# Optimization experiments

Measured on AMD Instinct MI355X. Metric: run time of the kernel, lower is better.

## Reference

```python
import jax, jax.numpy as jnp
import numpy as np

B = 32768
PASSES = 4

# mask layout: (batch, digit, row, col), values in {0,1}

def _to_lines(m, d):
    """Reorder so the last axis enumerates the 9 cells of a line and axis -2 the 9 lines."""
    if d == 'h':
        return m                      # lines = rows, cells = cols
    if d == 'v':
        return jnp.swapaxes(m, 2, 3)  # lines = cols, cells = rows
    b = m.shape[0]                    # lines = 3x3 boxes
    return m.reshape(b, 9, 3, 3, 3, 3).transpose(0, 1, 2, 4, 3, 5).reshape(b, 9, 9, 9)

_from_lines = _to_lines  # all three reorderings are self-inverse


def filter_line(m, d):
    """SudokuFilterHVBox: remove a solved cell's digit from all other cells in its line."""
    l = _to_lines(m, d)
    cnt = l.sum(axis=1, keepdims=True)                 # candidates per cell
    solved = l * (cnt == 1).astype(l.dtype)            # one-hot solved cells
    other = solved.sum(axis=-1, keepdims=True) - solved  # same digit solved elsewhere in line
    out = l * (other == 0).astype(l.dtype)
    return _from_lines(out, d)


def unique_line(m, d):
    """SudokuUniqueHVBox (hidden single): if a digit fits only one cell in a line, fix it."""
    l = _to_lines(m, d)
    cnt_line = l.sum(axis=-1, keepdims=True)           # per-digit count in the line
    hidden = l * (cnt_line == 1).astype(l.dtype)       # lone placements
    has = hidden.sum(axis=1, keepdims=True) > 0        # cell hosts a hidden single
    out = jnp.where(has, hidden, l)
    return _from_lines(out, d)


def doubles_line(m, d):
    """SudokuDigitsDoubles (naked pair): two identical 2-candidate cells in a line
    eliminate those digits from the rest of the line."""
    l = _to_lines(m, d)                                # (B, d, line, cell)
    cnt = l.sum(axis=1, keepdims=True)
    pm = l * (cnt == 2).astype(l.dtype)                # patterns of 2-candidate cells
    dot = jnp.einsum('bdlc,bdle->blce', pm, pm)        # pattern overlap between cells
    eye = jnp.eye(9, dtype=l.dtype)
    match = (dot == 2).astype(l.dtype) * (1.0 - eye)   # identical pair at another cell
    pairflag = match.sum(-1) > 0                       # (B, line, cell) part of a naked pair
    pair_digit = pm * pairflag[:, None, :, :].astype(l.dtype)
    total_pd = pair_digit.sum(-1, keepdims=True)       # digit belongs to some pair in line
    remove = (total_pd > 0) & (pair_digit == 0)
    out = l * (1.0 - remove.astype(l.dtype))
    return _from_lines(out, d)


def pointing(m, d):
    """SudokuDigitsInOneLineAtBox: if a digit's box candidates lie in one row/col,
    remove that digit from the rest of the row/col outside the box."""
    b = m.shape[0]
    v = m.reshape(b, 9, 3, 3, 3, 3)                    # (B, d, br, ri, bc, ci)
    if d == 'h':
        pres = v.sum(axis=5) > 0                       # (B,d,br,ri,bc) digit in row of box
        nrows = pres.sum(axis=3, keepdims=True)
        point = pres & (nrows == 1)                    # confined to single row within box
        tot = point.sum(axis=4, keepdims=True)         # over bc
        rem = (tot - point) > 0                        # pointing from another box hits us
        out = v * (1.0 - rem[..., None].astype(v.dtype))
    else:
        pres = v.sum(axis=3) > 0                       # (B,d,br,bc,ci) digit in col of box
        ncols = pres.sum(axis=4, keepdims=True)
        point = pres & (ncols == 1)
        tot = point.sum(axis=2, keepdims=True)         # over br
        rem = (tot - point) > 0
        out = v * (1.0 - rem[:, :, :, None, :, :].astype(v.dtype))
    return out.reshape(b, 9, 9, 9)


def _forward_mask(mask):
    for _ in range(PASSES):
        mask = filter_line(mask, 'box')
        mask = pointing(mask, 'h')
        mask = pointing(mask, 'v')
        mask = unique_line(mask, 'h')
        mask = unique_line(mask, 'v')
        mask = unique_line(mask, 'box')
        mask = doubles_line(mask, 'v')   # original code instantiates doubles_h with 'v'
        mask = doubles_line(mask, 'v')
        mask = doubles_line(mask, 'box')
    return mask


def setup_inputs() -> dict:
    key = jax.random.key(0)
    mask = jax.random.randint(key, (B, 9, 9, 9), 0, 2).astype(jnp.float32)
    return {"mask": mask}


def reference(mask):
    out = _forward_mask(mask)
    cnt = out.sum(axis=1)                              # candidates per cell
    solved = jnp.all(cnt == 1, axis=(1, 2))            # (B,) puzzle fully determined
    return (out, solved)
```

## Files before the change

kernel.cpp:

```cpp
#include <hip/hip_runtime.h>
#include <stdint.h>

#define NB 32768
#define NPASS 4
#define FULL27 0x07FFFFFFu
#define NBF (NB * 729)
#define PPW 16
#define NBLK (NB / PPW)
#define ROUNDS 183
#define POOLDW 368


__device__ __forceinline__ uint32_t colfold(uint32_t w) {
    return (w | (w >> 9) | (w >> 18)) & 0x1FFu;
}
__device__ __forceinline__ uint32_t colmaj2(uint32_t w) {
    return ((w & (w >> 9)) | ((w | (w >> 9)) & (w >> 18))) & 0x1FFu;
}
__device__ __forceinline__ uint32_t rotA(uint32_t v) {
    return (uint32_t)__builtin_amdgcn_update_dpp(0, (int)v, 0x09, 0xF, 0xF, true);
}
__device__ __forceinline__ uint32_t rotB(uint32_t v) {
    return (uint32_t)__builtin_amdgcn_update_dpp(0, (int)v, 0x12, 0xF, 0xF, true);
}

__global__ __launch_bounds__(64)
void sudoku_kernel(const uint32_t* __restrict__ in, float* __restrict__ out,
                   float* __restrict__ solved) {
    __shared__ uint32_t pool[POOLDW];
    const int lane = threadIdx.x;
    const int trip = lane >> 2;
    const int band = lane & 3;
    const int p0 = blockIdx.x * PPW;
    const int p = p0 + trip;

    {
        const int base = p0 * 729;
        #pragma unroll 1
        for (int c = 0; c < 11; ++c) {
            uint32_t v[16];
            #pragma unroll
            for (int j = 0; j < 16; ++j) {
                int gi = base + (c * 16 + j) * 64 + lane;
                if (gi >= NBF) gi = NBF - 1;
                v[j] = in[gi];
            }
            #pragma unroll
            for (int j = 0; j < 16; ++j) {
                unsigned long long m = __ballot(v[j] != 0u);
                if (lane == 0) {
                    int r = c * 16 + j;
                    pool[2 * r]     = (uint32_t)m;
                    pool[2 * r + 1] = (uint32_t)(m >> 32);
                }
            }
        }
        {
            uint32_t v[7];
            #pragma unroll
            for (int j = 0; j < 7; ++j) {
                int gi = base + (176 + j) * 64 + lane;
                if (gi >= NBF) gi = NBF - 1;
                v[j] = in[gi];
            }
            #pragma unroll
            for (int j = 0; j < 7; ++j) {
                unsigned long long m = __ballot(v[j] != 0u);
                if (lane == 0) {
                    int r = 176 + j;
                    pool[2 * r]     = (uint32_t)m;
                    pool[2 * r + 1] = (uint32_t)(m >> 32);
                }
            }
        }
    }
    __syncthreads();

    uint32_t bd[9];
    {
        const int bb0 = trip * 729 + band * 27;
        #pragma unroll
        for (int d = 0; d < 9; ++d) {
            int bb = bb0 + d * 81;
            int di = bb >> 5, sh = bb & 31;
            uint64_t both = (uint64_t)pool[di] | ((uint64_t)pool[di + 1] << 32);
            bd[d] = (uint32_t)(both >> sh) & FULL27;
        }
    }
    __syncthreads();

    #pragma unroll 1
    for (int pass = 0; pass < NPASS; ++pass) {
        {
            uint32_t on = 0, tw = 0, fo = 0;
            #pragma unroll
            for (int d = 0; d < 9; ++d) {
                uint32_t c = on & bd[d];
                on ^= bd[d]; fo |= tw & c; tw ^= c;
            }
            uint32_t ex1 = on & ~tw & ~fo;
            #pragma unroll
            for (int d = 0; d < 9; ++d) {
                uint32_t s = bd[d] & ex1;
                #pragma unroll
                for (int k = 0; k < 3; ++k) {
                    uint32_t bm = 0x1C0E07u << (3 * k);
                    uint32_t sm = s & bm;
                    uint32_t multi = sm & (sm - 1u);
                    uint32_t keep = (sm == 0u) ? 0xFFFFFFFFu : (~bm | (multi ? 0u : sm));
                    bd[d] &= keep;
                }
            }
        }

        #pragma unroll
        for (int d = 0; d < 9; ++d) {
            uint32_t w = bd[d];
            uint32_t t = (w | (w >> 1) | (w >> 2)) & 0x01249249u;
            uint32_t sum = (t & 0x1FFu) + ((t >> 9) & 0x1FFu) + ((t >> 18) & 0x1FFu);
            uint32_t single = sum & ~(sum >> 1) & 0x49u;
            uint32_t point = t & (single * 0x40201u);
            uint32_t clearm = 0;
            #pragma unroll
            for (int r = 0; r < 3; ++r) {
                uint32_t pr = (point >> (9 * r)) & 0x1FFu;
                uint32_t multi = pr & (pr - 1u);
                uint32_t segkeep = multi ? 0u : pr * 7u;
                uint32_t rc = pr ? ((0x1FFu & ~segkeep) << (9 * r)) : 0u;
                clearm |= rc;
            }
            bd[d] = w & ~clearm;
        }

        {
            uint32_t pnt[9];
            #pragma unroll
            for (int d = 0; d < 9; ++d) {
                uint32_t w = bd[d];
                uint32_t q = colfold(w);
                uint32_t u = (q & 0x49u) + ((q >> 1) & 0x49u) + ((q >> 2) & 0x49u);
                uint32_t single = u & ~(u >> 1) & 0x49u;
                pnt[d] = q & (single * 7u);
            }
            #pragma unroll
            for (int d = 0; d < 9; ++d) {
                uint32_t o = rotA(pnt[d]) | rotB(pnt[d]);
                bd[d] &= ~(o * 0x40201u);
            }
        }

        {
            uint32_t hid[9], has = 0;
            #pragma unroll
            for (int d = 0; d < 9; ++d) {
                uint32_t w = bd[d], h = 0;
                #pragma unroll
                for (int r = 0; r < 3; ++r) {
                    uint32_t x = w & (0x1FFu << (9 * r));
                    h |= (x & (x - 1u)) ? 0u : x;
                }
                hid[d] = h; has |= h;
            }
            #pragma unroll
            for (int d = 0; d < 9; ++d) bd[d] = (bd[d] & ~has) | hid[d];
        }

        {
            uint32_t hid[9], has = 0;
            #pragma unroll
            for (int d = 0; d < 9; ++d) {
                uint32_t w = bd[d];
                uint32_t q0 = colfold(w), m0 = colmaj2(w);
                uint32_t ex = q0 | (m0 << 9);
                uint32_t ea = rotA(ex);
                uint32_t eb = rotB(ex);
                uint32_t qa = ea & 0x1FFu, ma = ea >> 9;
                uint32_t qb = eb & 0x1FFu, mb = eb >> 9;
                uint32_t ge2 = m0 | ma | mb | (q0 & qa) | (q0 & qb) | (qa & qb);
                uint32_t ex1c = (q0 | qa | qb) & ~ge2;
                hid[d] = w & ((ex1c & q0) * 0x40201u);
                has |= hid[d];
            }
            #pragma unroll
            for (int d = 0; d < 9; ++d) bd[d] = (bd[d] & ~has) | hid[d];
        }

        {
            uint32_t hid[9], has = 0;
            #pragma unroll
            for (int d = 0; d < 9; ++d) {
                uint32_t w = bd[d], h = 0;
                #pragma unroll
                for (int k = 0; k < 3; ++k) {
                    uint32_t x = w & (0x1C0E07u << (3 * k));
                    h |= (x & (x - 1u)) ? 0u : x;
                }
                hid[d] = h; has |= h;
            }
            #pragma unroll
            for (int d = 0; d < 9; ++d) bd[d] = (bd[d] & ~has) | hid[d];
        }

        #pragma unroll 1
        for (int rep = 0; rep < 2; ++rep) {
            uint32_t on = 0, tw = 0, fo = 0;
            #pragma unroll
            for (int d = 0; d < 9; ++d) {
                uint32_t c = on & bd[d];
                on ^= bd[d]; fo |= tw & c; tw ^= c;
            }
            uint32_t ex2 = tw & ~on & ~fo;
            uint32_t Q[9], K[9];
            #pragma unroll
            for (int d = 0; d < 9; ++d) { Q[d] = bd[d] & ex2; K[d] = 0u; }
            #pragma unroll
            for (int d1 = 0; d1 < 9; ++d1)
                #pragma unroll
                for (int d2 = d1 + 1; d2 < 9; ++d2) {
                    uint32_t P = Q[d1] & Q[d2];
                    uint32_t f0 = colfold(P), g0 = colmaj2(P);
                    uint32_t ex = f0 | (g0 << 9);
                    uint32_t ea = rotA(ex);
                    uint32_t eb = rotB(ex);
                    uint32_t fa = ea & 0x1FFu, ga = ea >> 9;
                    uint32_t fb = eb & 0x1FFu, gb = eb >> 9;
                    uint32_t dup = g0 | ga | gb | (f0 & fa) | (f0 & fb) | (fa & fb);
                    uint32_t sK = P & (dup * 0x40201u);
                    K[d1] |= sK; K[d2] |= sK;
                }
            #pragma unroll
            for (int d = 0; d < 9; ++d) {
                uint32_t kc = colfold(K[d]);
                uint32_t cols = kc | rotA(kc) | rotB(kc);
                uint32_t em = cols * 0x40201u;
                bd[d] = (bd[d] & ~em) | K[d];
            }
        }

        {
            uint32_t on = 0, tw = 0, fo = 0;
            #pragma unroll
            for (int d = 0; d < 9; ++d) {
                uint32_t c = on & bd[d];
                on ^= bd[d]; fo |= tw & c; tw ^= c;
            }
            uint32_t ex2 = tw & ~on & ~fo;
            uint32_t Q[9], K[9];
            #pragma unroll
            for (int d = 0; d < 9; ++d) { Q[d] = bd[d] & ex2; K[d] = 0u; }
            #pragma unroll
            for (int d1 = 0; d1 < 9; ++d1)
                #pragma unroll
                for (int d2 = d1 + 1; d2 < 9; ++d2) {
                    uint32_t P = Q[d1] & Q[d2];
                    #pragma unroll
                    for (int k = 0; k < 3; ++k) {
                        uint32_t m = P & (0x1C0E07u << (3 * k));
                        uint32_t s = (m & (m - 1u)) ? m : 0u;
                        K[d1] |= s; K[d2] |= s;
                    }
                }
            #pragma unroll
            for (int d = 0; d < 9; ++d)
                #pragma unroll
                for (int k = 0; k < 3; ++k) {
                    uint32_t bm = 0x1C0E07u << (3 * k);
                    uint32_t t = K[d] & bm;
                    uint32_t mask = t ? (~bm | t) : 0xFFFFFFFFu;
                    bd[d] &= mask;
                }
        }
    }

    {
        uint32_t on = 0, tw = 0, fo = 0;
        #pragma unroll
        for (int d = 0; d < 9; ++d) {
            uint32_t c = on & bd[d];
            on ^= bd[d]; fo |= tw & c; tw ^= c;
        }
        uint32_t okb = ((on & ~tw & ~fo) == FULL27) ? 1u : 0u;
        uint32_t all = okb & rotA(okb) & rotB(okb);
        if (band == 0) solved[p] = all ? 1.0f : 0.0f;
    }

    for (int j = lane; j < POOLDW; j += 64) pool[j] = 0u;
    __syncthreads();
    if (band != 3) {
        const int pbit = trip * 729;
        #pragma unroll
        for (int d = 0; d < 9; ++d) {
            int bitbase = pbit + d * 81 + band * 27;
            int di = bitbase >> 5;
            int sh = bitbase & 31;
            uint64_t both = (uint64_t)bd[d] << sh;
            atomicOr(&pool[di], (uint32_t)both);
            atomicOr(&pool[di + 1], (uint32_t)(both >> 32));
        }
    }
    __syncthreads();
    {
        const int limit4 = PPW * 729 / 4;
        float4* dst4 = (float4*)(out + (size_t)p0 * 729);
        #pragma unroll 4
        for (int i = 0; i < 46; ++i) {
            int j = i * 64 + lane;
            if (j < limit4) {
                uint32_t nib = (pool[j >> 3] >> ((j & 7) * 4)) & 0xFu;
                dst4[j] = make_float4((float)(nib & 1u), (float)((nib >> 1) & 1u),
                                      (float)((nib >> 2) & 1u), (float)((nib >> 3) & 1u));
            }
        }
    }
}

extern "C" void kernel_launch(void* const* d_in, const int* in_sizes, int n_in,
                              void* d_out, int out_size, void* d_ws, size_t ws_size,
                              hipStream_t stream) {
    const uint32_t* in = (const uint32_t*)d_in[0];
    float* out = (float*)d_out;
    float* solved = out + (size_t)NB * 729;
    sudoku_kernel<<<NBLK, 64, 0, stream>>>(in, out, solved);
}
```

Before: 213.5 us.

## Split into bit-pack kernel and one-puzzle-per-lane solve kernel

Adds a separate pack kernel that reads the float mask with wide loads and packs it into a bitset workspace, so the input read is no longer done through per-block ballots. The solve kernel now gives each lane a whole puzzle, holding three bands in registers, which replaces the cross-lane DPP rotations with in-register indexing. Each lane now holds three times as much state, which raises register pressure and can limit occupancy. There are also only 512 blocks of 64 threads and a second kernel launch.

```diff
diff --git a/kernel.cpp b/kernel.cpp
--- a/kernel.cpp
+++ b/kernel.cpp
@@ -5,10 +5,11 @@
 #define NPASS 4
 #define FULL27 0x07FFFFFFu
 #define NBF (NB * 729)
-#define PPW 16
-#define NBLK (NB / PPW)
-#define ROUNDS 183
-#define POOLDW 368
+#define NWORDS (NBF / 32)
+#define PACK_BLKS (NWORDS / 256)
+#define SOLVE_PPB 64
+#define SOLVE_BLKS (NB / SOLVE_PPB)
+#define BLK_DW 1458
 
 
 __device__ __forceinline__ uint32_t colfold(uint32_t w) {
@@ -17,143 +18,124 @@
 __device__ __forceinline__ uint32_t colmaj2(uint32_t w) {
     return ((w & (w >> 9)) | ((w | (w >> 9)) & (w >> 18))) & 0x1FFu;
 }
-__device__ __forceinline__ uint32_t rotA(uint32_t v) {
-    return (uint32_t)__builtin_amdgcn_update_dpp(0, (int)v, 0x09, 0xF, 0xF, true);
-}
-__device__ __forceinline__ uint32_t rotB(uint32_t v) {
-    return (uint32_t)__builtin_amdgcn_update_dpp(0, (int)v, 0x12, 0xF, 0xF, true);
-}
-
-__global__ __launch_bounds__(64)
-void sudoku_kernel(const uint32_t* __restrict__ in, float* __restrict__ out,
-                   float* __restrict__ solved) {
-    __shared__ uint32_t pool[POOLDW];
+
+__global__ __launch_bounds__(256)
+void pack_kernel(const uint32_t* __restrict__ in, uint32_t* __restrict__ ws) {
+    const int g = blockIdx.x * 256 + threadIdx.x;
+    const uint4* src = (const uint4*)in + (size_t)g * 8;
+    uint32_t acc = 0u;
+    #pragma unroll
+    for (int j = 0; j < 8; ++j) {
+        uint4 v = src[j];
+        uint32_t n = ((v.x >> 23) & 1u) | (((v.y >> 23) & 1u) << 1)
+                   | (((v.z >> 23) & 1u) << 2) | (((v.w >> 23) & 1u) << 3);
+        acc |= n << (4 * j);
+    }
+    ws[g] = acc;
+}
+
+__global__ __launch_bounds__(64, 1)
+void solve_kernel(const uint32_t* __restrict__ ws, float* __restrict__ out,
+                  float* __restrict__ solved) {
+    __shared__ uint32_t lds[BLK_DW + 1];
     const int lane = threadIdx.x;
-    const int trip = lane >> 2;
-    const int band = lane & 3;
-    const int p0 = blockIdx.x * PPW;
-    const int p = p0 + trip;
-
-    {
-        const int base = p0 * 729;
-        #pragma unroll 1
-        for (int c = 0; c < 11; ++c) {
-            uint32_t v[16];
-            #pragma unroll
-            for (int j = 0; j < 16; ++j) {
-                int gi = base + (c * 16 + j) * 64 + lane;
-                if (gi >= NBF) gi = NBF - 1;
-                v[j] = in[gi];
-            }
-            #pragma unroll
-            for (int j = 0; j < 16; ++j) {
-                unsigned long long m = __ballot(v[j] != 0u);
-                if (lane == 0) {
-                    int r = c * 16 + j;
-                    pool[2 * r]     = (uint32_t)m;
-                    pool[2 * r + 1] = (uint32_t)(m >> 32);
-                }
-            }
-        }
-        {
-            uint32_t v[7];
-            #pragma unroll
-            for (int j = 0; j < 7; ++j) {
-                int gi = base + (176 + j) * 64 + lane;
-                if (gi >= NBF) gi = NBF - 1;
-                v[j] = in[gi];
-            }
-            #pragma unroll
-            for (int j = 0; j < 7; ++j) {
-                unsigned long long m = __ballot(v[j] != 0u);
-                if (lane == 0) {
-                    int r = 176 + j;
-                    pool[2 * r]     = (uint32_t)m;
-                    pool[2 * r + 1] = (uint32_t)(m >> 32);
-                }
-            }
+    const int P0 = blockIdx.x * SOLVE_PPB;
+
+    {
+        const uint2* wsrc = (const uint2*)(ws + (size_t)blockIdx.x * BLK_DW);
+        uint2* ldst = (uint2*)lds;
+        #pragma unroll
+        for (int i = 0; i < 12; ++i) {
+            int j = i * 64 + lane;
+            if (j < 729) ldst[j] = wsrc[j];
         }
     }
     __syncthreads();
 
-    uint32_t bd[9];
-    {
-        const int bb0 = trip * 729 + band * 27;
-        #pragma unroll
-        for (int d = 0; d < 9; ++d) {
-            int bb = bb0 + d * 81;
-            int di = bb >> 5, sh = bb & 31;
-            uint64_t both = (uint64_t)pool[di] | ((uint64_t)pool[di + 1] << 32);
-            bd[d] = (uint32_t)(both >> sh) & FULL27;
-        }
-    }
-    __syncthreads();
+    uint32_t bd[9][3];
+    {
+        const int qb = lane * 729;
+        #pragma unroll
+        for (int d = 0; d < 9; ++d)
+            #pragma unroll
+            for (int b = 0; b < 3; ++b) {
+                int bit = qb + d * 81 + b * 27;
+                int di = bit >> 5, sh = bit & 31;
+                uint64_t both = (uint64_t)lds[di] | ((uint64_t)lds[di + 1] << 32);
+                bd[d][b] = (uint32_t)(both >> sh) & FULL27;
+            }
+    }
 
     #pragma unroll 1
     for (int pass = 0; pass < NPASS; ++pass) {
-        {
+        #pragma unroll
+        for (int b = 0; b < 3; ++b) {
             uint32_t on = 0, tw = 0, fo = 0;
             #pragma unroll
             for (int d = 0; d < 9; ++d) {
-                uint32_t c = on & bd[d];
-                on ^= bd[d]; fo |= tw & c; tw ^= c;
+                uint32_t c = on & bd[d][b];
+                on ^= bd[d][b]; fo |= tw & c; tw ^= c;
             }
             uint32_t ex1 = on & ~tw & ~fo;
             #pragma unroll
             for (int d = 0; d < 9; ++d) {
-                uint32_t s = bd[d] & ex1;
+                uint32_t s = bd[d][b] & ex1;
                 #pragma unroll
                 for (int k = 0; k < 3; ++k) {
                     uint32_t bm = 0x1C0E07u << (3 * k);
                     uint32_t sm = s & bm;
                     uint32_t multi = sm & (sm - 1u);
                     uint32_t keep = (sm == 0u) ? 0xFFFFFFFFu : (~bm | (multi ? 0u : sm));
-                    bd[d] &= keep;
-                }
-            }
-        }
+                    bd[d][b] &= keep;
+                }
+            }
+        }
+
+        #pragma unroll
+        for (int b = 0; b < 3; ++b)
+            #pragma unroll
+            for (int d = 0; d < 9; ++d) {
+                uint32_t w = bd[d][b];
+                uint32_t t = (w | (w >> 1) | (w >> 2)) & 0x01249249u;
+                uint32_t sum = (t & 0x1FFu) + ((t >> 9) & 0x1FFu) + ((t >> 18) & 0x1FFu);
+                uint32_t single = sum & ~(sum >> 1) & 0x49u;
+                uint32_t point = t & (single * 0x40201u);
+                uint32_t clearm = 0;
+                #pragma unroll
+                for (int r = 0; r < 3; ++r) {
+                    uint32_t pr = (point >> (9 * r)) & 0x1FFu;
+                    uint32_t multi = pr & (pr - 1u);
+                    uint32_t segkeep = multi ? 0u : pr * 7u;
+                    uint32_t rc = pr ? ((0x1FFu & ~segkeep) << (9 * r)) : 0u;
+                    clearm |= rc;
+                }
+                bd[d][b] = w & ~clearm;
+            }
 
         #pragma unroll
         for (int d = 0; d < 9; ++d) {
-            uint32_t w = bd[d];
-            uint32_t t = (w | (w >> 1) | (w >> 2)) & 0x01249249u;
-            uint32_t sum = (t & 0x1FFu) + ((t >> 9) & 0x1FFu) + ((t >> 18) & 0x1FFu);
-            uint32_t single = sum & ~(sum >> 1) & 0x49u;
-            uint32_t point = t & (single * 0x40201u);
-            uint32_t clearm = 0;
-            #pragma unroll
-            for (int r = 0; r < 3; ++r) {
-                uint32_t pr = (point >> (9 * r)) & 0x1FFu;
-                uint32_t multi = pr & (pr - 1u);
-                uint32_t segkeep = multi ? 0u : pr * 7u;
-                uint32_t rc = pr ? ((0x1FFu & ~segkeep) << (9 * r)) : 0u;
-                clearm |= rc;
-            }
-            bd[d] = w & ~clearm;
-        }
-
-        {
-            uint32_t pnt[9];
-            #pragma unroll
-            for (int d = 0; d < 9; ++d) {
-                uint32_t w = bd[d];
+            uint32_t pn[3];
+            #pragma unroll
+            for (int b = 0; b < 3; ++b) {
+                uint32_t w = bd[d][b];
                 uint32_t q = colfold(w);
                 uint32_t u = (q & 0x49u) + ((q >> 1) & 0x49u) + ((q >> 2) & 0x49u);
                 uint32_t single = u & ~(u >> 1) & 0x49u;
-                pnt[d] = q & (single * 7u);
-            }
-            #pragma unroll
-            for (int d = 0; d < 9; ++d) {
-                uint32_t o = rotA(pnt[d]) | rotB(pnt[d]);
-                bd[d] &= ~(o * 0x40201u);
-            }
-        }
-
-        {
+                pn[b] = q & (single * 7u);
+            }
+            #pragma unroll
+            for (int b = 0; b < 3; ++b) {
+                uint32_t o = pn[(b + 1) % 3] | pn[(b + 2) % 3];
+                bd[d][b] &= ~(o * 0x40201u);
+            }
+        }
+
+        #pragma unroll
+        for (int b = 0; b < 3; ++b) {
             uint32_t hid[9], has = 0;
             #pragma unroll
             for (int d = 0; d < 9; ++d) {
-                uint32_t w = bd[d], h = 0;
+                uint32_t w = bd[d][b], h = 0;
                 #pragma unroll
                 for (int r = 0; r < 3; ++r) {
                     uint32_t x = w & (0x1FFu << (9 * r));
@@ -162,34 +144,41 @@
                 hid[d] = h; has |= h;
             }
             #pragma unroll
-            for (int d = 0; d < 9; ++d) bd[d] = (bd[d] & ~has) | hid[d];
+            for (int d = 0; d < 9; ++d) bd[d][b] = (bd[d][b] & ~has) | hid[d];
         }
 
         {
+            uint32_t hid[9][3], has[3] = {0u, 0u, 0u};
+            #pragma unroll
+            for (int d = 0; d < 9; ++d) {
+                uint32_t q[3], m[3];
+                #pragma unroll
+                for (int b = 0; b < 3; ++b) {
+                    q[b] = colfold(bd[d][b]);
+                    m[b] = colmaj2(bd[d][b]);
+                }
+                uint32_t ge2 = m[0] | m[1] | m[2]
+                             | (q[0] & q[1]) | (q[0] & q[2]) | (q[1] & q[2]);
+                uint32_t ex1c = (q[0] | q[1] | q[2]) & ~ge2;
+                #pragma unroll
+                for (int b = 0; b < 3; ++b) {
+                    hid[d][b] = bd[d][b] & ((ex1c & q[b]) * 0x40201u);
+                    has[b] |= hid[d][b];
+                }
+            }
+            #pragma unroll
+            for (int d = 0; d < 9; ++d)
+                #pragma unroll
+                for (int b = 0; b < 3; ++b)
+                    bd[d][b] = (bd[d][b] & ~has[b]) | hid[d][b];
+        }
+
+        #pragma unroll
+        for (int b = 0; b < 3; ++b) {
             uint32_t hid[9], has = 0;
             #pragma unroll
             for (int d = 0; d < 9; ++d) {
-                uint32_t w = bd[d];
-                uint32_t q0 = colfold(w), m0 = colmaj2(w);
-                uint32_t ex = q0 | (m0 << 9);
-                uint32_t ea = rotA(ex);
-                uint32_t eb = rotB(ex);
-                uint32_t qa = ea & 0x1FFu, ma = ea >> 9;
-                uint32_t qb = eb & 0x1FFu, mb = eb >> 9;
-                uint32_t ge2 = m0 | ma | mb | (q0 & qa) | (q0 & qb) | (qa & qb);
-                uint32_t ex1c = (q0 | qa | qb) & ~ge2;
-                hid[d] = w & ((ex1c & q0) * 0x40201u);
-                has |= hid[d];
-            }
-            #pragma unroll
-            for (int d = 0; d < 9; ++d) bd[d] = (bd[d] & ~has) | hid[d];
-        }
-
-        {
-            uint32_t hid[9], has = 0;
-            #pragma unroll
-            for (int d = 0; d < 9; ++d) {
-                uint32_t w = bd[d], h = 0;
+                uint32_t w = bd[d][b], h = 0;
                 #pragma unroll
                 for (int k = 0; k < 3; ++k) {
                     uint32_t x = w & (0x1C0E07u << (3 * k));
@@ -198,56 +187,69 @@
                 hid[d] = h; has |= h;
             }
             #pragma unroll
-            for (int d = 0; d < 9; ++d) bd[d] = (bd[d] & ~has) | hid[d];
+            for (int d = 0; d < 9; ++d) bd[d][b] = (bd[d][b] & ~has) | hid[d];
         }
 
         #pragma unroll 1
         for (int rep = 0; rep < 2; ++rep) {
+            uint32_t ex2[3];
+            #pragma unroll
+            for (int b = 0; b < 3; ++b) {
+                uint32_t on = 0, tw = 0, fo = 0;
+                #pragma unroll
+                for (int d = 0; d < 9; ++d) {
+                    uint32_t c = on & bd[d][b];
+                    on ^= bd[d][b]; fo |= tw & c; tw ^= c;
+                }
+                ex2[b] = tw & ~on & ~fo;
+            }
+            uint32_t Q[9][3], K[9][3];
+            #pragma unroll
+            for (int d = 0; d < 9; ++d)
+                #pragma unroll
+                for (int b = 0; b < 3; ++b) { Q[d][b] = bd[d][b] & ex2[b]; K[d][b] = 0u; }
+            #pragma unroll
+            for (int d1 = 0; d1 < 9; ++d1)
+                #pragma unroll
+                for (int d2 = d1 + 1; d2 < 9; ++d2) {
+                    uint32_t P[3], f[3], g[3];
+                    #pragma unroll
+                    for (int b = 0; b < 3; ++b) {
+                        P[b] = Q[d1][b] & Q[d2][b];
+                        f[b] = colfold(P[b]);
+                        g[b] = colmaj2(P[b]);
+                    }
+                    uint32_t dup = g[0] | g[1] | g[2]
+                                 | (f[0] & f[1]) | (f[0] & f[2]) | (f[1] & f[2]);
+                    uint32_t em = dup * 0x40201u;
+                    #pragma unroll
+                    for (int b = 0; b < 3; ++b) {
+                        uint32_t sK = P[b] & em;
+                        K[d1][b] |= sK; K[d2][b] |= sK;
+                    }
+                }
+            #pragma unroll
+            for (int d = 0; d < 9; ++d) {
+                uint32_t kc0 = colfold(K[d][0]), kc1 = colfold(K[d][1]), kc2 = colfold(K[d][2]);
+                uint32_t em = (kc0 | kc1 | kc2) * 0x40201u;
+                #pragma unroll
+                for (int b = 0; b < 3; ++b)
+                    bd[d][b] = (bd[d][b] & ~em) | K[d][b];
+            }
+        }
+
+        #pragma unroll
+        for (int b = 0; b < 3; ++b) {
             uint32_t on = 0, tw = 0, fo = 0;
             #pragma unroll
             for (int d = 0; d < 9; ++d) {
-                uint32_t c = on & bd[d];
-                on ^= bd[d]; fo |= tw & c; tw ^= c;
+                uint32_t c = on & bd[d][b];
+                on ^= bd[d][b]; fo |= tw & c; tw ^= c;
             }
             uint32_t ex2 = tw & ~on & ~fo;
             uint32_t Q[9], K[9];
             #pragma unroll
-            for (int d = 0; d < 9; ++d) { Q[d] = bd[d] & ex2; K[d] = 0u; }
-            #pragma unroll
-            for (int d1 = 0; d1 < 9; ++d1)
-                #pragma unroll
-                for (int d2 = d1 + 1; d2 < 9; ++d2) {
-                    uint32_t P = Q[d1] & Q[d2];
-                    uint32_t f0 = colfold(P), g0 = colmaj2(P);
-                    uint32_t ex = f0 | (g0 << 9);
-                    uint32_t ea = rotA(ex);
-                    uint32_t eb = rotB(ex);
-                    uint32_t fa = ea & 0x1FFu, ga = ea >> 9;
-                    uint32_t fb = eb & 0x1FFu, gb = eb >> 9;
-                    uint32_t dup = g0 | ga | gb | (f0 & fa) | (f0 & fb) | (fa & fb);
-                    uint32_t sK = P & (dup * 0x40201u);
-                    K[d1] |= sK; K[d2] |= sK;
-                }
-            #pragma unroll
-            for (int d = 0; d < 9; ++d) {
-                uint32_t kc = colfold(K[d]);
-                uint32_t cols = kc | rotA(kc) | rotB(kc);
-                uint32_t em = cols * 0x40201u;
-                bd[d] = (bd[d] & ~em) | K[d];
-            }
-        }
-
-        {
-            uint32_t on = 0, tw = 0, fo = 0;
-            #pragma unroll
-            for (int d = 0; d < 9; ++d) {
-                uint32_t c = on & bd[d];
-                on ^= bd[d]; fo |= tw & c; tw ^= c;
-            }
-            uint32_t ex2 = tw & ~on & ~fo;
-            uint32_t Q[9], K[9];
-            #pragma unroll
-            for (int d = 0; d < 9; ++d) { Q[d] = bd[d] & ex2; K[d] = 0u; }
+            for (int d = 0; d < 9; ++d) { Q[d] = bd[d][b] & ex2; K[d] = 0u; }
             #pragma unroll
             for (int d1 = 0; d1 < 9; ++d1)
                 #pragma unroll
@@ -267,46 +269,50 @@
                     uint32_t bm = 0x1C0E07u << (3 * k);
                     uint32_t t = K[d] & bm;
                     uint32_t mask = t ? (~bm | t) : 0xFFFFFFFFu;
-                    bd[d] &= mask;
-                }
-        }
-    }
-
-    {
-        uint32_t on = 0, tw = 0, fo = 0;
-        #pragma unroll
-        for (int d = 0; d < 9; ++d) {
-            uint32_t c = on & bd[d];
-            on ^= bd[d]; fo |= tw & c; tw ^= c;
-        }
-        uint32_t okb = ((on & ~tw & ~fo) == FULL27) ? 1u : 0u;
-        uint32_t all = okb & rotA(okb) & rotB(okb);
-        if (band == 0) solved[p] = all ? 1.0f : 0.0f;
-    }
-
-    for (int j = lane; j < POOLDW; j += 64) pool[j] = 0u;
+                    bd[d][b] &= mask;
+                }
+        }
+    }
+
+    {
+        uint32_t ok = 1u;
+        #pragma unroll
+        for (int b = 0; b < 3; ++b) {
+            uint32_t on = 0, tw = 0, fo = 0;
+            #pragma unroll
+            for (int d = 0; d < 9; ++d) {
+                uint32_t c = on & bd[d][b];
+                on ^= bd[d][b]; fo |= tw & c; tw ^= c;
+            }
+            ok &= ((on & ~tw & ~fo) == FULL27) ? 1u : 0u;
+        }
+        solved[P0 + lane] = ok ? 1.0f : 0.0f;
+    }
+
     __syncthreads();
-    if (band != 3) {
-        const int pbit = trip * 729;
-        #pragma unroll
-        for (int d = 0; d < 9; ++d) {
-            int bitbase = pbit + d * 81 + band * 27;
-            int di = bitbase >> 5;
-            int sh = bitbase & 31;
-            uint64_t both = (uint64_t)bd[d] << sh;
-            atomicOr(&pool[di], (uint32_t)both);
-            atomicOr(&pool[di + 1], (uint32_t)(both >> 32));
-        }
-    }
+    for (int j = lane; j < BLK_DW + 1; j += 64) lds[j] = 0u;
     __syncthreads();
     {
-        const int limit4 = PPW * 729 / 4;
-        float4* dst4 = (float4*)(out + (size_t)p0 * 729);
+        const int qb = lane * 729;
+        #pragma unroll
+        for (int d = 0; d < 9; ++d)
+            #pragma unroll
+            for (int b = 0; b < 3; ++b) {
+                int bit = qb + d * 81 + b * 27;
+                int di = bit >> 5, sh = bit & 31;
+                uint64_t both = (uint64_t)bd[d][b] << sh;
+                atomicOr(&lds[di], (uint32_t)both);
+                atomicOr(&lds[di + 1], (uint32_t)(both >> 32));
+            }
+    }
+    __syncthreads();
+    {
+        float4* dst4 = (float4*)(out + (size_t)P0 * 729);
         #pragma unroll 4
-        for (int i = 0; i < 46; ++i) {
+        for (int i = 0; i < 183; ++i) {
             int j = i * 64 + lane;
-            if (j < limit4) {
-                uint32_t nib = (pool[j >> 3] >> ((j & 7) * 4)) & 0xFu;
+            if (j < 11664) {
+                uint32_t nib = (lds[j >> 3] >> ((j & 7) * 4)) & 0xFu;
                 dst4[j] = make_float4((float)(nib & 1u), (float)((nib >> 1) & 1u),
                                       (float)((nib >> 2) & 1u), (float)((nib >> 3) & 1u));
             }
@@ -320,5 +326,8 @@
     const uint32_t* in = (const uint32_t*)d_in[0];
     float* out = (float*)d_out;
     float* solved = out + (size_t)NB * 729;
-    sudoku_kernel<<<NBLK, 64, 0, stream>>>(in, out, solved);
-}
+    uint32_t* ws = (uint32_t*)d_ws;
+
+    pack_kernel<<<PACK_BLKS, 256, 0, stream>>>(in, ws);
+    solve_kernel<<<SOLVE_BLKS, 64, 0, stream>>>(ws, out, solved);
+}
```

New measurement: 241.6 us. 13.2% more time.

## Split input bit-packing into separate pack kernel and widen solver blocks

Applied to the files above, without the earlier changes.

Adds a pack kernel that reads the float mask with 128-bit loads and packs the exponent bit (nonzero test for 0/1 floats) into a bitmask workspace. The solver then reads the packed words into LDS with 64-bit loads, in blocks of 256 threads holding 64 puzzles instead of 64-thread blocks of 16. This removes the per-element ballot loop and the serialized lane-0 LDS writes from the solver. The cost is a second launch and a round trip of the packed mask through global memory. The bit-23 test assumes inputs are exactly 0.0 or 1.0.

```diff
diff --git a/kernel.cpp b/kernel.cpp
--- a/kernel.cpp
+++ b/kernel.cpp
@@ -5,10 +5,11 @@
 #define NPASS 4
 #define FULL27 0x07FFFFFFu
 #define NBF (NB * 729)
-#define PPW 16
-#define NBLK (NB / PPW)
-#define ROUNDS 183
-#define POOLDW 368
+#define NWORDS (NBF / 32)
+#define PACK_BLKS (NWORDS / 256)
+#define PUZ_PER_BLK 64
+#define SOLVE_BLKS (NB / PUZ_PER_BLK)
+#define BLK_DW 1458
 
 
 __device__ __forceinline__ uint32_t colfold(uint32_t w) {
@@ -24,66 +25,49 @@
     return (uint32_t)__builtin_amdgcn_update_dpp(0, (int)v, 0x12, 0xF, 0xF, true);
 }
 
-__global__ __launch_bounds__(64)
-void sudoku_kernel(const uint32_t* __restrict__ in, float* __restrict__ out,
-                   float* __restrict__ solved) {
-    __shared__ uint32_t pool[POOLDW];
-    const int lane = threadIdx.x;
-    const int trip = lane >> 2;
-    const int band = lane & 3;
-    const int p0 = blockIdx.x * PPW;
-    const int p = p0 + trip;
+__global__ __launch_bounds__(256)
+void pack_kernel(const uint32_t* __restrict__ in, uint32_t* __restrict__ ws) {
+    const int g = blockIdx.x * 256 + threadIdx.x;
+    const uint4* src = (const uint4*)in + (size_t)g * 8;
+    uint32_t acc = 0u;
+    #pragma unroll
+    for (int j = 0; j < 8; ++j) {
+        uint4 v = src[j];
+        uint32_t n = ((v.x >> 23) & 1u) | (((v.y >> 23) & 1u) << 1)
+                   | (((v.z >> 23) & 1u) << 2) | (((v.w >> 23) & 1u) << 3);
+        acc |= n << (4 * j);
+    }
+    ws[g] = acc;
+}
+
+__global__ __launch_bounds__(256)
+void solve_kernel(const uint32_t* __restrict__ ws, float* __restrict__ out,
+                  float* __restrict__ solved) {
+    __shared__ uint32_t lds[BLK_DW + 2];
+    const int tid = threadIdx.x;
+    const int q = tid >> 2;
+    const int band = tid & 3;
+    const int P0 = blockIdx.x * PUZ_PER_BLK;
 
     {
-        const int base = p0 * 729;
-        #pragma unroll 1
-        for (int c = 0; c < 11; ++c) {
-            uint32_t v[16];
-            #pragma unroll
-            for (int j = 0; j < 16; ++j) {
-                int gi = base + (c * 16 + j) * 64 + lane;
-                if (gi >= NBF) gi = NBF - 1;
-                v[j] = in[gi];
-            }
-            #pragma unroll
-            for (int j = 0; j < 16; ++j) {
-                unsigned long long m = __ballot(v[j] != 0u);
-                if (lane == 0) {
-                    int r = c * 16 + j;
-                    pool[2 * r]     = (uint32_t)m;
-                    pool[2 * r + 1] = (uint32_t)(m >> 32);
-                }
-            }
-        }
-        {
-            uint32_t v[7];
-            #pragma unroll
-            for (int j = 0; j < 7; ++j) {
-                int gi = base + (176 + j) * 64 + lane;
-                if (gi >= NBF) gi = NBF - 1;
-                v[j] = in[gi];
-            }
-            #pragma unroll
-            for (int j = 0; j < 7; ++j) {
-                unsigned long long m = __ballot(v[j] != 0u);
-                if (lane == 0) {
-                    int r = 176 + j;
-                    pool[2 * r]     = (uint32_t)m;
-                    pool[2 * r + 1] = (uint32_t)(m >> 32);
-                }
-            }
+        const uint2* wsrc = (const uint2*)(ws + (size_t)blockIdx.x * BLK_DW);
+        uint2* ldst = (uint2*)lds;
+        #pragma unroll
+        for (int i = 0; i < 3; ++i) {
+            int j = i * 256 + tid;
+            if (j < 729) ldst[j] = wsrc[j];
         }
     }
     __syncthreads();
 
     uint32_t bd[9];
     {
-        const int bb0 = trip * 729 + band * 27;
+        const int bb0 = q * 729 + band * 27;
         #pragma unroll
         for (int d = 0; d < 9; ++d) {
-            int bb = bb0 + d * 81;
-            int di = bb >> 5, sh = bb & 31;
-            uint64_t both = (uint64_t)pool[di] | ((uint64_t)pool[di + 1] << 32);
+            int bit = bb0 + d * 81;
+            int di = bit >> 5, sh = bit & 31;
+            uint64_t both = (uint64_t)lds[di] | ((uint64_t)lds[di + 1] << 32);
             bd[d] = (uint32_t)(both >> sh) & FULL27;
         }
     }
@@ -137,10 +121,10 @@
             #pragma unroll
             for (int d = 0; d < 9; ++d) {
                 uint32_t w = bd[d];
-                uint32_t q = colfold(w);
-                uint32_t u = (q & 0x49u) + ((q >> 1) & 0x49u) + ((q >> 2) & 0x49u);
+                uint32_t qq = colfold(w);
+                uint32_t u = (qq & 0x49u) + ((qq >> 1) & 0x49u) + ((qq >> 2) & 0x49u);
                 uint32_t single = u & ~(u >> 1) & 0x49u;
-                pnt[d] = q & (single * 7u);
+                pnt[d] = qq & (single * 7u);
             }
             #pragma unroll
             for (int d = 0; d < 9; ++d) {
@@ -281,32 +265,31 @@
         }
         uint32_t okb = ((on & ~tw & ~fo) == FULL27) ? 1u : 0u;
         uint32_t all = okb & rotA(okb) & rotB(okb);
-        if (band == 0) solved[p] = all ? 1.0f : 0.0f;
-    }
-
-    for (int j = lane; j < POOLDW; j += 64) pool[j] = 0u;
+        if (band == 0) solved[P0 + q] = all ? 1.0f : 0.0f;
+    }
+
+    for (int j = tid; j < BLK_DW + 2; j += 256) lds[j] = 0u;
     __syncthreads();
     if (band != 3) {
-        const int pbit = trip * 729;
+        const int pbit = q * 729;
         #pragma unroll
         for (int d = 0; d < 9; ++d) {
             int bitbase = pbit + d * 81 + band * 27;
             int di = bitbase >> 5;
             int sh = bitbase & 31;
             uint64_t both = (uint64_t)bd[d] << sh;
-            atomicOr(&pool[di], (uint32_t)both);
-            atomicOr(&pool[di + 1], (uint32_t)(both >> 32));
+            atomicOr(&lds[di], (uint32_t)both);
+            atomicOr(&lds[di + 1], (uint32_t)(both >> 32));
         }
     }
     __syncthreads();
     {
-        const int limit4 = PPW * 729 / 4;
-        float4* dst4 = (float4*)(out + (size_t)p0 * 729);
+        float4* dst4 = (float4*)(out + (size_t)P0 * 729);
         #pragma unroll 4
         for (int i = 0; i < 46; ++i) {
-            int j = i * 64 + lane;
-            if (j < limit4) {
-                uint32_t nib = (pool[j >> 3] >> ((j & 7) * 4)) & 0xFu;
+            int j = i * 256 + tid;
+            if (j < 11664) {
+                uint32_t nib = (lds[j >> 3] >> ((j & 7) * 4)) & 0xFu;
                 dst4[j] = make_float4((float)(nib & 1u), (float)((nib >> 1) & 1u),
                                       (float)((nib >> 2) & 1u), (float)((nib >> 3) & 1u));
             }
@@ -320,5 +303,8 @@
     const uint32_t* in = (const uint32_t*)d_in[0];
     float* out = (float*)d_out;
     float* solved = out + (size_t)NB * 729;
-    sudoku_kernel<<<NBLK, 64, 0, stream>>>(in, out, solved);
-}
+    uint32_t* ws = (uint32_t*)d_ws;
+
+    pack_kernel<<<PACK_BLKS, 256, 0, stream>>>(in, ws);
+    solve_kernel<<<SOLVE_BLKS, 256, 0, stream>>>(ws, out, solved);
+}
```

Measured after the change: 216.2 us. Within noise of the previous version (+1.3%).
